# Performance work log

Hardware: AMD Instinct MI355X
Metric: run time of the kernel (lower is better)

Reference implementation:

```python
import jax, jax.numpy as jnp
import numpy as np

N = 4096      # nodes
E = 131072    # edges (avg degree 32)
C = 256       # in/hidden channels
NC = 10       # classes
RATIO = 0.5
DEPTH = 2


def _build_adj(edge_index, w, n):
    # COO -> dense, duplicate edges summed (matches CSR coalescing)
    A = jnp.zeros((n, n), jnp.float32)
    return A.at[edge_index[0], edge_index[1]].add(w)


def _gcn(x, A, W, b, fill=2.0):
    # gcn_norm with improved=True: add_remaining_self_loops(fill=2.0),
    # deg from target (col) sums, sym norm; out[i] = sum_j Anorm[j,i] * (xW)[j]
    n = A.shape[0]
    idx = jnp.arange(n)
    diag = A[idx, idx]
    A = A.at[idx, idx].set(jnp.where(diag != 0, diag, fill))
    deg = A.sum(axis=0)
    dinv = jnp.where(deg > 0, jax.lax.rsqrt(deg), 0.0)
    An = dinv[:, None] * A * dinv[None, :]
    return An.T @ (x @ W) + b


def _augment(A):
    # remove_self_loops + add_self_loops(weight 1) == set diag to 1,
    # then adj @ adj, then remove self loops again
    n = A.shape[0]
    idx = jnp.arange(n)
    A = A.at[idx, idx].set(1.0)
    A2 = A @ A
    return A2.at[idx, idx].set(0.0)


def _pool(x, A, p, k):
    # TopKPooling: score = tanh(x.p / ||p||), keep top-k nodes, gate x by score
    score = jnp.tanh((x @ p) / jnp.linalg.norm(p))
    vals, perm = jax.lax.top_k(score, k)
    x2 = x[perm] * vals[:, None]
    A2 = A[perm][:, perm]   # filter_adj: keep edges with both ends selected
    return x2, A2


def reference(x, edge_index, w0, b0, w1, b1, w2, b2, p1, p2, wc, bc):
    A = _build_adj(edge_index, jnp.ones((edge_index.shape[1],), x.dtype), x.shape[0])
    x = jax.nn.relu(_gcn(x, A, w0, b0))
    k = x.shape[0]
    for (W, b, p) in ((w1, b1, p1), (w2, b2, p2)):
        A = _augment(A)
        k = int(np.ceil(RATIO * k))  # static per level (single graph)
        x, A = _pool(x, A, p, k)
        x = jax.nn.relu(_gcn(x, A, W, b))
    emb = x.mean(axis=0, keepdims=True)                      # global_mean_pool, batch all-zero
    emb = emb / jnp.maximum(jnp.linalg.norm(emb, axis=-1, keepdims=True), 1e-12)
    logits = emb @ wc.T + bc
    return emb, jax.nn.log_softmax(logits, axis=1)


def setup_inputs() -> dict:
    key = jax.random.key(0)
    ks = jax.random.split(key, 12)
    s = 1.0 / np.sqrt(C)
    return {
        'x': jax.random.normal(ks[0], (N, C), jnp.float32),
        'edge_index': jax.random.randint(ks[1], (2, E), 0, N, jnp.int64) if jax.config.jax_enable_x64 else jax.random.randint(ks[1], (2, E), 0, N, jnp.int32),
        'w0': jax.random.normal(ks[2], (C, C), jnp.float32) * s,
        'b0': jnp.zeros((C,), jnp.float32),
        'w1': jax.random.normal(ks[3], (C, C), jnp.float32) * s,
        'b1': jnp.zeros((C,), jnp.float32),
        'w2': jax.random.normal(ks[4], (C, C), jnp.float32) * s,
        'b2': jnp.zeros((C,), jnp.float32),
        'p1': jax.random.normal(ks[5], (C,), jnp.float32) * s,
        'p2': jax.random.normal(ks[6], (C,), jnp.float32) * s,
        'wc': jax.random.normal(ks[7], (NC, C), jnp.float32) * s,
        'bc': jnp.zeros((NC,), jnp.float32),
    }
```

## Files before the change

### kernel.cpp

```cpp
#include <hip/hip_runtime.h>
#include <math.h>

#define CH 256

typedef short short8 __attribute__((ext_vector_type(8)));
typedef float f32x4 __attribute__((ext_vector_type(4)));

__device__ inline ushort f2bf(float f) {
  unsigned u = __float_as_uint(f);
  unsigned r = (u + 0x7FFFu + ((u >> 16) & 1u)) >> 16;
  return (ushort)r;
}

__device__ inline void gload16(const void* g, void* l) {
  __builtin_amdgcn_global_load_lds((const __attribute__((address_space(1))) void*)g,
                                   (__attribute__((address_space(3))) void*)l, 16, 0, 0);
}


__global__ void scatter_edges(const int* __restrict__ ei, int E, int n, float* __restrict__ A) {
  int e = blockIdx.x * blockDim.x + threadIdx.x;
  if (e < E) atomicAdd(&A[(size_t)ei[e] * n + ei[E + e]], 1.0f);
}

template <int DIAGMODE>
__global__ __launch_bounds__(256) void transpose_deg(const float* __restrict__ In, int n,
                                                     ushort* __restrict__ O, float* __restrict__ deg,
                                                     int zn, size_t zoff) {
  __shared__ float t[64][65];
  int j0 = blockIdx.x * 64, i0 = blockIdx.y * 64;
  int tx = threadIdx.x & 63, ty4 = threadIdx.x >> 6;
  float s = 0.f;
#pragma unroll
  for (int r = 0; r < 64; r += 4) {
    int gi = i0 + ty4 + r, gj = j0 + tx;
    size_t idx = (size_t)gi * n + gj;
    float v = In[idx];
    for (int z = 1; z < zn; ++z) v += In[idx + (size_t)z * zoff];
    if (gi == gj) v = (DIAGMODE == 1) ? 2.0f : ((v != 0.f) ? v : 2.0f);
    t[ty4 + r][tx] = v;
    s += v;
  }
  atomicAdd(&deg[j0 + tx], s);
  __syncthreads();
#pragma unroll
  for (int r = 0; r < 64; r += 4) {
    int c = ty4 + r;
    O[(size_t)(j0 + c) * n + i0 + tx] = f2bf(t[tx][c]);
  }
}

__global__ __launch_bounds__(256) void topk_rank(const float* __restrict__ sc, int n, int k,
                                                 int* __restrict__ perm, float* __restrict__ vals) {
  extern __shared__ unsigned long long kbuf[];
  __shared__ int red[4][64];
  int tid = threadIdx.x;
  for (int i = tid; i < n; i += 256) {
    unsigned u = __float_as_uint(sc[i]);
    u = (u & 0x80000000u) ? ~u : (u | 0x80000000u);
    kbuf[i] = ((unsigned long long)u << 32) | (0xFFFFFFFFu - (unsigned)i);
  }
  __syncthreads();
  const int ti = tid & 63, tj = tid >> 6;
  const int i = blockIdx.x * 64 + ti;
  const unsigned long long ki = kbuf[i];
  int cnt = 0;
  const int q = n >> 2;
  const int jb = tj * q, je = jb + q;
#pragma unroll 4
  for (int j = jb; j < je; j += 2) {
    unsigned long long k0 = kbuf[j], k1 = kbuf[j + 1];
    cnt += (k0 > ki) + (k1 > ki);
  }
  red[tj][ti] = cnt;
  __syncthreads();
  if (tid < 64) {
    int r = red[0][ti] + red[1][ti] + red[2][ti] + red[3][ti];
    if (r < k) { perm[r] = i; vals[r] = sc[i]; }
  }
}

__global__ void pool_x(const float* __restrict__ x, const int* __restrict__ perm,
                       const float* __restrict__ vals, float* __restrict__ xo) {
  int i = blockIdx.x, c = threadIdx.x;
  xo[(size_t)i * CH + c] = x[(size_t)perm[i] * CH + c] * vals[i];
}


__global__ void rowgather_cvt(const float* __restrict__ A, const int* __restrict__ perm,
                              int n, ushort* __restrict__ O) {
  int m = blockIdx.y;
  int src = perm[m];
  int k4 = (blockIdx.x * 256 + threadIdx.x) * 4;
  float4 v = *(const float4*)&A[(size_t)src * n + k4];
  if (src >= k4 && src < k4 + 4) ((float*)&v)[src - k4] = 1.0f;
  ushort4 o;
  o.x = f2bf(v.x); o.y = f2bf(v.y); o.z = f2bf(v.z); o.w = f2bf(v.w);
  *(ushort4*)&O[(size_t)m * n + k4] = o;
}

__global__ void rowgather_bf16(const ushort* __restrict__ At, const int* __restrict__ perm,
                               int n, ushort* __restrict__ O) {
  int m = blockIdx.y;
  int src = perm[m];
  int k8 = (blockIdx.x * 256 + threadIdx.x) * 8;
  uint4 v = *(const uint4*)&At[(size_t)src * n + k8];
  if (src >= k8 && src < k8 + 8) ((ushort*)&v)[src - k8] = 0x3F80;
  *(uint4*)&O[(size_t)m * n + k8] = v;
}


__device__ inline void stage_tile(const ushort* ag, const ushort* bg, int ktOff,
                                  char* asb, char* bsb, int K) {
#pragma unroll
  for (int i = 0; i < 4; ++i)
    gload16(ag + (size_t)i * 32 * K + ktOff, asb + i * 4096);
#pragma unroll
  for (int i = 0; i < 4; ++i)
    gload16(bg + (size_t)i * 32 * K + ktOff, bsb + i * 4096);
}

__device__ inline void compute_tile(const ushort (*__restrict__ As)[64],
                                    const ushort (*__restrict__ Bs)[64],
                                    int wm, int wn, int lrow, int col0, int col1,
                                    f32x4 acc[4][4]) {
#pragma unroll
  for (int ks = 0; ks < 2; ++ks) {
    const int col = ks ? col1 : col0;
    short8 af[4], bf[4];
#pragma unroll
    for (int t = 0; t < 4; ++t)
      af[t] = *(const short8*)&As[wm + t * 16 + lrow][col];
#pragma unroll
    for (int t = 0; t < 4; ++t)
      bf[t] = *(const short8*)&Bs[wn + t * 16 + lrow][col];
#pragma unroll
    for (int mt = 0; mt < 4; ++mt)
#pragma unroll
      for (int nt = 0; nt < 4; ++nt)
        acc[mt][nt] = __builtin_amdgcn_mfma_f32_16x16x32_bf16(af[mt], bf[nt], acc[mt][nt], 0, 0, 0);
  }
}

__global__ __launch_bounds__(256) void mfma_nt(const ushort* __restrict__ Aop,
                                               const ushort* __restrict__ Bop,
                                               float* __restrict__ C, int ldc,
                                               int K, int Ks, size_t zstride) {
  __shared__ ushort As[3][128][64];
  __shared__ ushort Bs[3][128][64];
  const int tid = threadIdx.x;
  const int wave = tid >> 6, lane = tid & 63;
  const int wm = (wave & 1) * 64, wn = (wave >> 1) * 64;
  const int m0 = blockIdx.x * 128, n0 = blockIdx.y * 128;
  const int k0 = blockIdx.z * Ks;
  C += (size_t)blockIdx.z * zstride;
  const int lrow = lane & 15;
  const int q = lane >> 4;
  const int rx = lane & 7;
  const int col0 = ((q)     ^ rx) * 8;
  const int col1 = ((4 + q) ^ rx) * 8;
  const int srow = wave * 8 + (lane >> 3);
  const int scol = ((lane & 7) ^ (lane >> 3)) * 8;
  const ushort* ag = Aop + (size_t)(m0 + srow) * K + k0 + scol;
  const ushort* bg = Bop + (size_t)(n0 + srow) * K + k0 + scol;
  f32x4 acc[4][4] = {};

  const int nk = Ks >> 6;

#define STAGE(bi, idx) stage_tile(ag, bg, (idx) * 64, \
    (char*)&As[bi][0][0] + wave * 1024, (char*)&Bs[bi][0][0] + wave * 1024, K)

  STAGE(0, 0);
  if (1 < nk) STAGE(1, 1);
  if (2 < nk) STAGE(2, 2);

  int bi = 0;
  for (int t = 0; t < nk - 2; ++t) {
    asm volatile("s_waitcnt vmcnt(16)" ::: "memory");
    __builtin_amdgcn_s_barrier();
    __builtin_amdgcn_sched_barrier(0);
    compute_tile(As[bi], Bs[bi], wm, wn, lrow, col0, col1, acc);
    __builtin_amdgcn_sched_barrier(0);
    __builtin_amdgcn_s_barrier();
    if (t + 3 < nk) STAGE(bi, t + 3);
    bi = (bi + 1 < 3) ? bi + 1 : 0;
  }
  asm volatile("s_waitcnt vmcnt(8)" ::: "memory");
  __builtin_amdgcn_s_barrier();
  __builtin_amdgcn_sched_barrier(0);
  compute_tile(As[bi], Bs[bi], wm, wn, lrow, col0, col1, acc);
  bi = (bi + 1 < 3) ? bi + 1 : 0;
  asm volatile("s_waitcnt vmcnt(0)" ::: "memory");
  __builtin_amdgcn_s_barrier();
  __builtin_amdgcn_sched_barrier(0);
  compute_tile(As[bi], Bs[bi], wm, wn, lrow, col0, col1, acc);
#undef STAGE

  const int crow = (lane >> 4) * 4, ccol = lane & 15;
#pragma unroll
  for (int mt = 0; mt < 4; ++mt)
#pragma unroll
    for (int nt = 0; nt < 4; ++nt) {
      int gm = m0 + wm + mt * 16 + crow;
      int gn = n0 + wn + nt * 16 + ccol;
#pragma unroll
      for (int r = 0; r < 4; ++r)
        C[(size_t)(gm + r) * ldc + gn] = acc[mt][nt][r];
    }
}

__global__ void agg_epilogue(const float* __restrict__ Cred, size_t zstride, int zn,
                             const float* __restrict__ deg,
                             const float* __restrict__ bias, float* __restrict__ xo,
                             const float* __restrict__ p, float* __restrict__ sc) {
  int idx = blockIdx.x * 256 + threadIdx.x;
  int c4 = idx & 63;
  int m = idx >> 6;
  float d = deg[m];
  float s = (d > 0.f) ? 1.0f / sqrtf(d) : 0.f;
  float4 v = ((const float4*)Cred)[idx];
  for (int z = 1; z < zn; ++z) {
    float4 u = ((const float4*)(Cred + (size_t)z * zstride))[idx];
    v.x += u.x; v.y += u.y; v.z += u.z; v.w += u.w;
  }
  float4 b = ((const float4*)bias)[c4];
  v.x = fmaxf(fmaf(v.x, s, b.x), 0.f);
  v.y = fmaxf(fmaf(v.y, s, b.y), 0.f);
  v.z = fmaxf(fmaf(v.z, s, b.z), 0.f);
  v.w = fmaxf(fmaf(v.w, s, b.w), 0.f);
  ((float4*)xo)[idx] = v;
  if (p) {
    float4 pv = ((const float4*)p)[c4];
    float dot = v.x * pv.x + v.y * pv.y + v.z * pv.z + v.w * pv.w;
    float pn  = pv.x * pv.x + pv.y * pv.y + pv.z * pv.z + pv.w * pv.w;
    for (int off = 32; off; off >>= 1) {
      dot += __shfl_down(dot, off);
      pn  += __shfl_down(pn, off);
    }
    if ((threadIdx.x & 63) == 0) sc[m] = tanhf(dot / sqrtf(pn));
  }
}

__global__ __launch_bounds__(256) void xw_gemm(const float* __restrict__ Am,
                                               const float* __restrict__ Bm,
                                               ushort* __restrict__ Gt,
                                               int M, const float* __restrict__ deg) {
  __shared__ float As[16][64];
  __shared__ float Bs[16][64];
  const int tid = threadIdx.x;
  const int m0 = blockIdx.x * 64, n0 = blockIdx.y * 64;
  float acc[4][4] = {{0.f}};
  const int tm = tid & 15, tn = tid >> 4;

  for (int kt = 0; kt < CH; kt += 16) {
    __syncthreads();
    {
      int mm = tid >> 2, kq = (tid & 3) * 4;
      float4 v = *(const float4*)(Am + (size_t)(m0 + mm) * CH + kt + kq);
      As[kq + 0][mm] = v.x; As[kq + 1][mm] = v.y; As[kq + 2][mm] = v.z; As[kq + 3][mm] = v.w;
    }
#pragma unroll
    for (int r = 0; r < 4; ++r) {
      int idx = tid + r * 256;
      int kk = idx >> 6, nn = idx & 63;
      Bs[kk][nn] = Bm[(size_t)(kt + kk) * CH + (n0 + nn)];
    }
    __syncthreads();
#pragma unroll
    for (int kk = 0; kk < 16; ++kk) {
      float4 a = *(const float4*)&As[kk][tm * 4];
      float4 b = *(const float4*)&Bs[kk][tn * 4];
      acc[0][0] = fmaf(a.x, b.x, acc[0][0]);
      acc[0][1] = fmaf(a.x, b.y, acc[0][1]);
      acc[0][2] = fmaf(a.x, b.z, acc[0][2]);
      acc[0][3] = fmaf(a.x, b.w, acc[0][3]);
      acc[1][0] = fmaf(a.y, b.x, acc[1][0]);
      acc[1][1] = fmaf(a.y, b.y, acc[1][1]);
      acc[1][2] = fmaf(a.y, b.z, acc[1][2]);
      acc[1][3] = fmaf(a.y, b.w, acc[1][3]);
      acc[2][0] = fmaf(a.z, b.x, acc[2][0]);
      acc[2][1] = fmaf(a.z, b.y, acc[2][1]);
      acc[2][2] = fmaf(a.z, b.z, acc[2][2]);
      acc[2][3] = fmaf(a.z, b.w, acc[2][3]);
      acc[3][0] = fmaf(a.w, b.x, acc[3][0]);
      acc[3][1] = fmaf(a.w, b.y, acc[3][1]);
      acc[3][2] = fmaf(a.w, b.z, acc[3][2]);
      acc[3][3] = fmaf(a.w, b.w, acc[3][3]);
    }
  }

#pragma unroll
  for (int ii = 0; ii < 4; ++ii) {
    int m = m0 + tm * 4 + ii;
    float d = deg[m];
    float s = (d > 0.f) ? 1.0f / sqrtf(d) : 0.f;
#pragma unroll
    for (int jj = 0; jj < 4; ++jj) {
      int n = n0 + tn * 4 + jj;
      Gt[(size_t)n * M + m] = f2bf(s * acc[ii][jj]);
    }
  }
}


__global__ void mean_partial(const float* __restrict__ x2, float* __restrict__ macc) {
  int c = threadIdx.x;
  int j0 = blockIdx.x * 16;
  float s = 0.f;
#pragma unroll
  for (int j = 0; j < 16; ++j) s += x2[(size_t)(j0 + j) * CH + c];
  atomicAdd(&macc[c], s);
}

__global__ __launch_bounds__(256) void finalize2(const float* __restrict__ macc, int nr,
                                                 const float* __restrict__ wc,
                                                 const float* __restrict__ bc,
                                                 float* __restrict__ out) {
  __shared__ float semb[256];
  __shared__ float red[256];
  __shared__ float slog[16];
  int c = threadIdx.x;
  float emb = macc[c] / (float)nr;
  red[c] = emb * emb;
  __syncthreads();
  for (int off = 128; off; off >>= 1) {
    if (c < off) red[c] += red[c + off];
    __syncthreads();
  }
  float denom = fmaxf(sqrtf(red[0]), 1e-12f);
  float en = emb / denom;
  semb[c] = en;
  out[c] = en;
  __syncthreads();
  if (c < 10) {
    float l = bc[c];
    for (int t = 0; t < CH; ++t) l = fmaf(semb[t], wc[c * CH + t], l);
    slog[c] = l;
  }
  __syncthreads();
  if (c == 0) {
    float mx = slog[0];
    for (int j = 1; j < 10; ++j) mx = fmaxf(mx, slog[j]);
    float se = 0.f;
    for (int j = 0; j < 10; ++j) se += expf(slog[j] - mx);
    float lse = mx + logf(se);
    for (int j = 0; j < 10; ++j) out[CH + j] = slog[j] - lse;
  }
}


extern "C" void kernel_launch(void* const* d_in, const int* in_sizes, int n_in,
                              void* d_out, int out_size, void* d_ws, size_t ws_size,
                              hipStream_t stream) {
  const float* x  = (const float*)d_in[0];
  const int*   ei = (const int*)d_in[1];
  const float* w0 = (const float*)d_in[2];
  const float* b0 = (const float*)d_in[3];
  const float* w1 = (const float*)d_in[4];
  const float* b1 = (const float*)d_in[5];
  const float* w2 = (const float*)d_in[6];
  const float* b2 = (const float*)d_in[7];
  const float* p1 = (const float*)d_in[8];
  const float* p2 = (const float*)d_in[9];
  const float* wc = (const float*)d_in[10];
  const float* bc = (const float*)d_in[11];
  float* out = (float*)d_out;
  const int N0 = 4096, K1 = 2048, K2 = 1024;
  int E = in_sizes[1] / 2;

  float* W = (float*)d_ws;
  size_t off = 0;
  float* A    = W + off; off += (size_t)N0 * N0;
  float* Pa   = W + off; off += (size_t)K1 * K1;
  ushort* At  = (ushort*)(W + off); off += (size_t)N0 * N0 / 2;
  ushort* Arow = (ushort*)(W + off); off += (size_t)K1 * N0 / 2;
  ushort* Brow = (ushort*)A;
  float* Paux = A + (size_t)8 * 1024 * 1024;
  float* Cred = (float*)Arow;
  float* x0   = W + off; off += (size_t)N0 * CH;
  ushort* Gt  = (ushort*)(W + off); off += (size_t)N0 * CH / 2;
  float* xp  = W + off; off += (size_t)K1 * CH;
  float* x1  = W + off; off += (size_t)K1 * CH;
  float* x2  = W + off; off += (size_t)K2 * CH;
  float* sc  = W + off; off += 4096;
  float* vals = W + off; off += 4096;
  float* deg  = W + off; off += 4096;
  float* macc = W + off; off += 256;
  int* perm1 = (int*)(W + off); off += 4096;
  int* perm2 = (int*)(W + off); off += 4096;

  hipMemsetAsync(A, 0, (size_t)N0 * N0 * 4, stream);
  scatter_edges<<<(E + 255) / 256, 256, 0, stream>>>(ei, E, N0, A);

  hipMemsetAsync(deg, 0, N0 * 4, stream);
  transpose_deg<0><<<dim3(N0 / 64, N0 / 64), 256, 0, stream>>>(A, N0, At, deg, 1, 0);
  xw_gemm<<<dim3(N0 / 64, CH / 64), 256, 0, stream>>>(x, w0, Gt, N0, deg);
  mfma_nt<<<dim3(N0 / 128, CH / 128, 4), 256, 0, stream>>>(At, Gt, Cred, CH, N0, N0 / 4, (size_t)N0 * CH);
  agg_epilogue<<<N0 / 4, 256, 0, stream>>>(Cred, (size_t)N0 * CH, 4, deg, b0, x0, p1, sc);

  topk_rank<<<N0 / 64, 256, N0 * 8, stream>>>(sc, N0, K1, perm1, vals);

  rowgather_cvt<<<dim3(N0 / 1024, K1), 256, 0, stream>>>(A, perm1, N0, Arow);
  rowgather_bf16<<<dim3(N0 / 2048, K1), 256, 0, stream>>>(At, perm1, N0, Brow);
  mfma_nt<<<dim3(K1 / 128, K1 / 128, 1), 256, 0, stream>>>(Arow, Brow, Pa, K1, N0, N0, 0);
  pool_x<<<K1, 256, 0, stream>>>(x0, perm1, vals, xp);

  hipMemsetAsync(deg, 0, K1 * 4, stream);
  transpose_deg<1><<<dim3(K1 / 64, K1 / 64), 256, 0, stream>>>(Pa, K1, At, deg, 1, 0);
  xw_gemm<<<dim3(K1 / 64, CH / 64), 256, 0, stream>>>(xp, w1, Gt, K1, deg);
  mfma_nt<<<dim3(K1 / 128, CH / 128, 8), 256, 0, stream>>>(At, Gt, Cred, CH, K1, K1 / 8, (size_t)K1 * CH);
  agg_epilogue<<<K1 / 4, 256, 0, stream>>>(Cred, (size_t)K1 * CH, 8, deg, b1, x1, p2, sc);

  topk_rank<<<K1 / 64, 256, K1 * 8, stream>>>(sc, K1, K2, perm2, vals);

  rowgather_cvt<<<dim3(K1 / 1024, K2), 256, 0, stream>>>(Pa, perm2, K1, Arow);
  rowgather_bf16<<<dim3(K1 / 2048, K2), 256, 0, stream>>>(At, perm2, K1, Brow);
  mfma_nt<<<dim3(K2 / 128, K2 / 128, 4), 256, 0, stream>>>(Arow, Brow, Paux, K2, K1, K1 / 4, (size_t)K2 * K2);
  pool_x<<<K2, 256, 0, stream>>>(x1, perm2, vals, xp);

  hipMemsetAsync(deg, 0, K2 * 4, stream);
  transpose_deg<1><<<dim3(K2 / 64, K2 / 64), 256, 0, stream>>>(Paux, K2, At, deg, 4, (size_t)K2 * K2);
  xw_gemm<<<dim3(K2 / 64, CH / 64), 256, 0, stream>>>(xp, w2, Gt, K2, deg);
  mfma_nt<<<dim3(K2 / 128, CH / 128, 8), 256, 0, stream>>>(At, Gt, Cred, CH, K2, K2 / 8, (size_t)K2 * CH);
  agg_epilogue<<<K2 / 4, 256, 0, stream>>>(Cred, (size_t)K2 * CH, 8, deg, b2, x2, nullptr, nullptr);

  hipMemsetAsync(macc, 0, 256 * 4, stream);
  mean_partial<<<K2 / 16, 256, 0, stream>>>(x2, macc);
  finalize2<<<1, 256, 0, stream>>>(macc, K2, wc, bc, out);
}
```

Baseline: 427.6 us.

## Template GEMM tile width and add split-K for the augmentation GEMMs

Makes the MFMA GEMM kernel generic over the N tile width. The feature-aggregation GEMMs use 64-wide tiles so they launch twice as many blocks. The BN=128 variant uses a two-stage LDS pipeline instead of three. The pooled-adjacency GEMMs are now split along K (2 and 8 slices), and the partial results are summed inside transpose_deg and a z-loop added to rowgather_cvt. The aim is to fill more CUs on these small grids, at the cost of extra partial-sum memory traffic and reduction reads.

```diff
diff --git a/kernel.cpp b/kernel.cpp
--- a/kernel.cpp
+++ b/kernel.cpp
@@ -86,13 +86,16 @@
   xo[(size_t)i * CH + c] = x[(size_t)perm[i] * CH + c] * vals[i];
 }
 
-
 __global__ void rowgather_cvt(const float* __restrict__ A, const int* __restrict__ perm,
-                              int n, ushort* __restrict__ O) {
+                              int n, ushort* __restrict__ O, int zn, size_t zoff) {
   int m = blockIdx.y;
   int src = perm[m];
   int k4 = (blockIdx.x * 256 + threadIdx.x) * 4;
   float4 v = *(const float4*)&A[(size_t)src * n + k4];
+  for (int z = 1; z < zn; ++z) {
+    float4 u = *(const float4*)&A[(size_t)z * zoff + (size_t)src * n + k4];
+    v.x += u.x; v.y += u.y; v.z += u.z; v.w += u.w;
+  }
   if (src >= k4 && src < k4 + 4) ((float*)&v)[src - k4] = 1.0f;
   ushort4 o;
   o.x = f2bf(v.x); o.y = f2bf(v.y); o.z = f2bf(v.z); o.w = f2bf(v.w);
@@ -110,48 +113,53 @@
 }
 
 
+template <int BN>
 __device__ inline void stage_tile(const ushort* ag, const ushort* bg, int ktOff,
                                   char* asb, char* bsb, int K) {
 #pragma unroll
   for (int i = 0; i < 4; ++i)
     gload16(ag + (size_t)i * 32 * K + ktOff, asb + i * 4096);
 #pragma unroll
-  for (int i = 0; i < 4; ++i)
+  for (int i = 0; i < BN / 32; ++i)
     gload16(bg + (size_t)i * 32 * K + ktOff, bsb + i * 4096);
 }
 
+template <int BN>
 __device__ inline void compute_tile(const ushort (*__restrict__ As)[64],
                                     const ushort (*__restrict__ Bs)[64],
                                     int wm, int wn, int lrow, int col0, int col1,
-                                    f32x4 acc[4][4]) {
+                                    f32x4 acc[4][BN / 32]) {
 #pragma unroll
   for (int ks = 0; ks < 2; ++ks) {
     const int col = ks ? col1 : col0;
-    short8 af[4], bf[4];
+    short8 af[4], bf[BN / 32];
 #pragma unroll
     for (int t = 0; t < 4; ++t)
       af[t] = *(const short8*)&As[wm + t * 16 + lrow][col];
 #pragma unroll
-    for (int t = 0; t < 4; ++t)
+    for (int t = 0; t < BN / 32; ++t)
       bf[t] = *(const short8*)&Bs[wn + t * 16 + lrow][col];
 #pragma unroll
     for (int mt = 0; mt < 4; ++mt)
 #pragma unroll
-      for (int nt = 0; nt < 4; ++nt)
+      for (int nt = 0; nt < BN / 32; ++nt)
         acc[mt][nt] = __builtin_amdgcn_mfma_f32_16x16x32_bf16(af[mt], bf[nt], acc[mt][nt], 0, 0, 0);
   }
 }
 
+template <int BN>
 __global__ __launch_bounds__(256) void mfma_nt(const ushort* __restrict__ Aop,
                                                const ushort* __restrict__ Bop,
                                                float* __restrict__ C, int ldc,
                                                int K, int Ks, size_t zstride) {
-  __shared__ ushort As[3][128][64];
-  __shared__ ushort Bs[3][128][64];
+  constexpr int NBUF = (BN == 128) ? 2 : 3;
+  constexpr int NT = BN / 32;
+  __shared__ ushort As[NBUF][128][64];
+  __shared__ ushort Bs[NBUF][BN][64];
   const int tid = threadIdx.x;
   const int wave = tid >> 6, lane = tid & 63;
-  const int wm = (wave & 1) * 64, wn = (wave >> 1) * 64;
-  const int m0 = blockIdx.x * 128, n0 = blockIdx.y * 128;
+  const int wm = (wave & 1) * 64, wn = (wave >> 1) * (BN / 2);
+  const int m0 = blockIdx.x * 128, n0 = blockIdx.y * BN;
   const int k0 = blockIdx.z * Ks;
   C += (size_t)blockIdx.z * zstride;
   const int lrow = lane & 15;
@@ -163,44 +171,63 @@
   const int scol = ((lane & 7) ^ (lane >> 3)) * 8;
   const ushort* ag = Aop + (size_t)(m0 + srow) * K + k0 + scol;
   const ushort* bg = Bop + (size_t)(n0 + srow) * K + k0 + scol;
-  f32x4 acc[4][4] = {};
+  f32x4 acc[4][NT] = {};
 
   const int nk = Ks >> 6;
 
-#define STAGE(bi, idx) stage_tile(ag, bg, (idx) * 64, \
+#define STAGE(bi, idx) stage_tile<BN>(ag, bg, (idx) * 64, \
     (char*)&As[bi][0][0] + wave * 1024, (char*)&Bs[bi][0][0] + wave * 1024, K)
 
-  STAGE(0, 0);
-  if (1 < nk) STAGE(1, 1);
-  if (2 < nk) STAGE(2, 2);
-
-  int bi = 0;
-  for (int t = 0; t < nk - 2; ++t) {
-    asm volatile("s_waitcnt vmcnt(16)" ::: "memory");
+  if constexpr (NBUF == 2) {
+    STAGE(0, 0);
+    if (1 < nk) STAGE(1, 1);
+    int bi = 0;
+    for (int t = 0; t < nk - 1; ++t) {
+      asm volatile("s_waitcnt vmcnt(8)" ::: "memory");
+      __builtin_amdgcn_s_barrier();
+      __builtin_amdgcn_sched_barrier(0);
+      compute_tile<BN>(As[bi], Bs[bi], wm, wn, lrow, col0, col1, acc);
+      __builtin_amdgcn_sched_barrier(0);
+      __builtin_amdgcn_s_barrier();
+      if (t + 2 < nk) STAGE(bi, t + 2);
+      bi ^= 1;
+    }
+    asm volatile("s_waitcnt vmcnt(0)" ::: "memory");
     __builtin_amdgcn_s_barrier();
     __builtin_amdgcn_sched_barrier(0);
-    compute_tile(As[bi], Bs[bi], wm, wn, lrow, col0, col1, acc);
+    compute_tile<BN>(As[bi], Bs[bi], wm, wn, lrow, col0, col1, acc);
+  } else {
+    STAGE(0, 0);
+    if (1 < nk) STAGE(1, 1);
+    if (2 < nk) STAGE(2, 2);
+    int bi = 0;
+    for (int t = 0; t < nk - 2; ++t) {
+      asm volatile("s_waitcnt vmcnt(12)" ::: "memory");
+      __builtin_amdgcn_s_barrier();
+      __builtin_amdgcn_sched_barrier(0);
+      compute_tile<BN>(As[bi], Bs[bi], wm, wn, lrow, col0, col1, acc);
+      __builtin_amdgcn_sched_barrier(0);
+      __builtin_amdgcn_s_barrier();
+      if (t + 3 < nk) STAGE(bi, t + 3);
+      bi = (bi + 1 < 3) ? bi + 1 : 0;
+    }
+    asm volatile("s_waitcnt vmcnt(6)" ::: "memory");
+    __builtin_amdgcn_s_barrier();
     __builtin_amdgcn_sched_barrier(0);
+    compute_tile<BN>(As[bi], Bs[bi], wm, wn, lrow, col0, col1, acc);
+    bi = (bi + 1 < 3) ? bi + 1 : 0;
+    asm volatile("s_waitcnt vmcnt(0)" ::: "memory");
     __builtin_amdgcn_s_barrier();
-    if (t + 3 < nk) STAGE(bi, t + 3);
-    bi = (bi + 1 < 3) ? bi + 1 : 0;
-  }
-  asm volatile("s_waitcnt vmcnt(8)" ::: "memory");
-  __builtin_amdgcn_s_barrier();
-  __builtin_amdgcn_sched_barrier(0);
-  compute_tile(As[bi], Bs[bi], wm, wn, lrow, col0, col1, acc);
-  bi = (bi + 1 < 3) ? bi + 1 : 0;
-  asm volatile("s_waitcnt vmcnt(0)" ::: "memory");
-  __builtin_amdgcn_s_barrier();
-  __builtin_amdgcn_sched_barrier(0);
-  compute_tile(As[bi], Bs[bi], wm, wn, lrow, col0, col1, acc);
+    __builtin_amdgcn_sched_barrier(0);
+    compute_tile<BN>(As[bi], Bs[bi], wm, wn, lrow, col0, col1, acc);
+  }
 #undef STAGE
 
   const int crow = (lane >> 4) * 4, ccol = lane & 15;
 #pragma unroll
   for (int mt = 0; mt < 4; ++mt)
 #pragma unroll
-    for (int nt = 0; nt < 4; ++nt) {
+    for (int nt = 0; nt < NT; ++nt) {
       int gm = m0 + wm + mt * 16 + crow;
       int gn = n0 + wn + nt * 16 + ccol;
 #pragma unroll
@@ -388,6 +415,7 @@
   float* macc = W + off; off += 256;
   int* perm1 = (int*)(W + off); off += 4096;
   int* perm2 = (int*)(W + off); off += 4096;
+  (void)Pa;
 
   hipMemsetAsync(A, 0, (size_t)N0 * N0 * 4, stream);
   scatter_edges<<<(E + 255) / 256, 256, 0, stream>>>(ei, E, N0, A);
@@ -395,33 +423,33 @@
   hipMemsetAsync(deg, 0, N0 * 4, stream);
   transpose_deg<0><<<dim3(N0 / 64, N0 / 64), 256, 0, stream>>>(A, N0, At, deg, 1, 0);
   xw_gemm<<<dim3(N0 / 64, CH / 64), 256, 0, stream>>>(x, w0, Gt, N0, deg);
-  mfma_nt<<<dim3(N0 / 128, CH / 128, 4), 256, 0, stream>>>(At, Gt, Cred, CH, N0, N0 / 4, (size_t)N0 * CH);
+  mfma_nt<64><<<dim3(N0 / 128, CH / 64, 4), 256, 0, stream>>>(At, Gt, Cred, CH, N0, N0 / 4, (size_t)N0 * CH);
   agg_epilogue<<<N0 / 4, 256, 0, stream>>>(Cred, (size_t)N0 * CH, 4, deg, b0, x0, p1, sc);
 
   topk_rank<<<N0 / 64, 256, N0 * 8, stream>>>(sc, N0, K1, perm1, vals);
 
-  rowgather_cvt<<<dim3(N0 / 1024, K1), 256, 0, stream>>>(A, perm1, N0, Arow);
+  rowgather_cvt<<<dim3(N0 / 1024, K1), 256, 0, stream>>>(A, perm1, N0, Arow, 1, 0);
   rowgather_bf16<<<dim3(N0 / 2048, K1), 256, 0, stream>>>(At, perm1, N0, Brow);
-  mfma_nt<<<dim3(K1 / 128, K1 / 128, 1), 256, 0, stream>>>(Arow, Brow, Pa, K1, N0, N0, 0);
+  mfma_nt<128><<<dim3(K1 / 128, K1 / 128, 2), 256, 0, stream>>>(Arow, Brow, Paux, K1, N0, N0 / 2, (size_t)K1 * K1);
   pool_x<<<K1, 256, 0, stream>>>(x0, perm1, vals, xp);
 
   hipMemsetAsync(deg, 0, K1 * 4, stream);
-  transpose_deg<1><<<dim3(K1 / 64, K1 / 64), 256, 0, stream>>>(Pa, K1, At, deg, 1, 0);
+  transpose_deg<1><<<dim3(K1 / 64, K1 / 64), 256, 0, stream>>>(Paux, K1, At, deg, 2, (size_t)K1 * K1);
   xw_gemm<<<dim3(K1 / 64, CH / 64), 256, 0, stream>>>(xp, w1, Gt, K1, deg);
-  mfma_nt<<<dim3(K1 / 128, CH / 128, 8), 256, 0, stream>>>(At, Gt, Cred, CH, K1, K1 / 8, (size_t)K1 * CH);
+  mfma_nt<64><<<dim3(K1 / 128, CH / 64, 8), 256, 0, stream>>>(At, Gt, Cred, CH, K1, K1 / 8, (size_t)K1 * CH);
   agg_epilogue<<<K1 / 4, 256, 0, stream>>>(Cred, (size_t)K1 * CH, 8, deg, b1, x1, p2, sc);
 
   topk_rank<<<K1 / 64, 256, K1 * 8, stream>>>(sc, K1, K2, perm2, vals);
 
-  rowgather_cvt<<<dim3(K1 / 1024, K2), 256, 0, stream>>>(Pa, perm2, K1, Arow);
+  rowgather_cvt<<<dim3(K1 / 1024, K2), 256, 0, stream>>>(Paux, perm2, K1, Arow, 2, (size_t)K1 * K1);
   rowgather_bf16<<<dim3(K1 / 2048, K2), 256, 0, stream>>>(At, perm2, K1, Brow);
-  mfma_nt<<<dim3(K2 / 128, K2 / 128, 4), 256, 0, stream>>>(Arow, Brow, Paux, K2, K1, K1 / 4, (size_t)K2 * K2);
+  mfma_nt<128><<<dim3(K2 / 128, K2 / 128, 8), 256, 0, stream>>>(Arow, Brow, Paux, K2, K1, K1 / 8, (size_t)K2 * K2);
   pool_x<<<K2, 256, 0, stream>>>(x1, perm2, vals, xp);
 
   hipMemsetAsync(deg, 0, K2 * 4, stream);
-  transpose_deg<1><<<dim3(K2 / 64, K2 / 64), 256, 0, stream>>>(Paux, K2, At, deg, 4, (size_t)K2 * K2);
+  transpose_deg<1><<<dim3(K2 / 64, K2 / 64), 256, 0, stream>>>(Paux, K2, At, deg, 8, (size_t)K2 * K2);
   xw_gemm<<<dim3(K2 / 64, CH / 64), 256, 0, stream>>>(xp, w2, Gt, K2, deg);
-  mfma_nt<<<dim3(K2 / 128, CH / 128, 8), 256, 0, stream>>>(At, Gt, Cred, CH, K2, K2 / 8, (size_t)K2 * CH);
+  mfma_nt<64><<<dim3(K2 / 128, CH / 64, 8), 256, 0, stream>>>(At, Gt, Cred, CH, K2, K2 / 8, (size_t)K2 * CH);
   agg_epilogue<<<K2 / 4, 256, 0, stream>>>(Cred, (size_t)K2 * CH, 8, deg, b2, x2, nullptr, nullptr);
 
   hipMemsetAsync(macc, 0, 256 * 4, stream);
```

New measurement: 423.6 us. No clear change (-0.9%).
